# Optimization experiments

Measured on AMD Instinct MI355X. Metric: run time of the kernel, lower is better.

Reference implementation:

```python
import jax, jax.numpy as jnp
import numpy as np

B, C, H, W = 4, 512, 96, 96
NH = 8
HD = C // NH
NC = 128
D = 768
L = H * W
EPS = 1e-5  # torch LayerNorm default


def _l2n(x, axis):
    # F.normalize: x / max(||x||, 1e-12)
    return x / jnp.maximum(jnp.linalg.norm(x, axis=axis, keepdims=True), 1e-12)


def _ln2d(x, g, b):
    # LayerNorm2d: normalize over channel dim of (B,C,H,W)
    mu = x.mean(1, keepdims=True)
    var = ((x - mu) ** 2).mean(1, keepdims=True)
    return (x - mu) / jnp.sqrt(var + EPS) * g[None, :, None, None] + b[None, :, None, None]


def _conv1x1(x, w):
    return jnp.einsum('oc,bchw->bohw', w, x)


def setup_inputs() -> dict:
    key = jax.random.key(0)
    ks = jax.random.split(key, 9)
    s = 0.02
    return {
        'img_feats': jax.random.normal(ks[0], (B, C, H, W), jnp.float32),
        'cls_embs': jax.random.normal(ks[1], (NC, D), jnp.float32),
        'cls_logits': jax.random.normal(ks[2], (B, NC), jnp.float32),
        'seg_logits': jax.random.normal(ks[3], (B, 1, H, W), jnp.float32),
        'gamma_g': jnp.ones((D,), jnp.float32), 'beta_g': jnp.zeros((D,), jnp.float32),
        'gamma_f': jnp.ones((C,), jnp.float32), 'beta_f': jnp.zeros((C,), jnp.float32),
        'attn_scale': jnp.ones((NH, 1, 1), jnp.float32),
        'Wg': jax.random.normal(ks[4], (C, D), jnp.float32) * s,
        'Wqkv': jax.random.normal(ks[5], (3 * C, C), jnp.float32) * s,
        'Wo': jax.random.normal(ks[6], (C, C), jnp.float32) * s,
        'bo': jnp.zeros((C,), jnp.float32),
        'gamma_n': jnp.ones((C,), jnp.float32), 'beta_n': jnp.zeros((C,), jnp.float32),
        'W1': jax.random.normal(ks[7], (C, C), jnp.float32) * s, 'b1': jnp.zeros((C,), jnp.float32),
        'W2': jax.random.normal(ks[8], (C, C), jnp.float32) * s, 'b2': jnp.zeros((C,), jnp.float32),
    }


def reference(img_feats, cls_embs, cls_logits, seg_logits, gamma_g, beta_g,
              gamma_f, beta_f, attn_scale, Wg, Wqkv, Wo, bo, gamma_n, beta_n,
              W1, b1, W2, b2):
    xn = _ln2d(img_feats, gamma_f, beta_f)
    # guide LayerNorm over embedding dim
    mu = cls_embs.mean(-1, keepdims=True)
    var = ((cls_embs - mu) ** 2).mean(-1, keepdims=True)
    cn = (cls_embs - mu) / jnp.sqrt(var + EPS) * gamma_g + beta_g
    g = (cn @ Wg.T).reshape(NC, NH, HD)  # nc nh hd

    qkv = _conv1x1(xn, Wqkv).reshape(B, 3, NH, HD, L)
    q, k, v = qkv[:, 0], qkv[:, 1], qkv[:, 2]  # each (B,NH,HD,L)

    # cosine guide map + min-max normalization + softmax-weighted aggregation over classes
    gm = jnp.einsum('nhd,bhdl->bhnl', _l2n(g, -1), _l2n(q, -2))
    gm = gm - gm.min(-1, keepdims=True)
    gm = gm / gm.max(-1, keepdims=True)
    gm = (jax.nn.softmax(gm, axis=2) * gm).sum(2, keepdims=True)  # (B,NH,1,L)

    # auxiliary guide map from cls logits + masked pooling of k
    cls_obj = jnp.einsum('nhd,bn->bhd', g, cls_logits)
    mask = jax.nn.sigmoid(seg_logits)  # (B,1,H,W)
    seg_obj = (mask * k.reshape(B, C, H, W)).sum((2, 3)) / mask.sum((2, 3))  # (B,C)
    obj = _l2n(cls_obj + seg_obj.reshape(B, NH, HD), -1)
    aux = jnp.einsum('bhd,bhdl->bhl', obj, _l2n(k, -2))[:, :, None, :]
    aux = aux - aux.min(-1, keepdims=True)
    aux = aux / aux.max(-1, keepdims=True)
    gm = gm * aux

    v = gm * v
    # channel (transposed) cosine attention: (B,NH,HD,HD)
    attn = jnp.einsum('bhdl,bhel->bhde', _l2n(q, -1), _l2n(k, -1)) * attn_scale
    out = jnp.einsum('bhde,bhel->bhdl', jax.nn.softmax(attn, -1), v).reshape(B, C, H, W)

    x = img_feats + _conv1x1(out, Wo) + bo[None, :, None, None]
    # ConvMlp with pre-norm: LayerNorm2d -> 1x1 conv -> GELU -> 1x1 conv
    fin = _ln2d(x, gamma_n, beta_n)
    h = jax.nn.gelu(_conv1x1(fin, W1) + b1[None, :, None, None], approximate=False)
    return x + _conv1x1(h, W2) + b2[None, :, None, None]
```

## Files before the change

### kernel.cpp

```cpp
#include <hip/hip_runtime.h>
#include <hip/hip_bf16.h>
#include <math.h>

#define BB 4
#define CC 512
#define NHEAD 8
#define HDIM 64
#define NCLS 128
#define DD 768
#define LL 9216
#define BLPIX 36864
#define EPSV 1e-5f
#define GMBLK 144
#define AUXBLK 144
#define LSPLIT 8
#define NLT 72

typedef __hip_bfloat16 bf16;
typedef __attribute__((ext_vector_type(8))) short short8v;
typedef __attribute__((ext_vector_type(4))) short short4v;
typedef __attribute__((ext_vector_type(4))) float f32x4;

__device__ __forceinline__ float bf2f(bf16 v){ return __bfloat162float(v); }
__device__ __forceinline__ bf16 f2bf(float v){ return __float2bfloat16(v); }
__device__ __forceinline__ short bfbits(float v){ bf16 b = __float2bfloat16(v); return *reinterpret_cast<short*>(&b); }
__device__ __forceinline__ float s2f(short s){ bf16 b = *reinterpret_cast<bf16*>(&s); return __bfloat162float(b); }

__global__ __launch_bounds__(256) void wclsg_k(
    const float* __restrict__ wqkv, const float* __restrict__ wo,
    const float* __restrict__ w1, const float* __restrict__ w2,
    bf16* __restrict__ oq, bf16* __restrict__ oo,
    bf16* __restrict__ o1, bf16* __restrict__ o2,
    const float* __restrict__ cls_embs, const float* __restrict__ gamma_g,
    const float* __restrict__ beta_g, const float* __restrict__ Wg,
    float* __restrict__ g, bf16* __restrict__ gnb)
{
  __shared__ __align__(16) float cn[DD];
  __shared__ float red[256];
  __shared__ float gsh[CC];
  __shared__ float nrm[NHEAD];
  int bid = blockIdx.x;
  int tid = threadIdx.x;
  if (bid < 1536){
    int i = bid * 256 + tid;
    int e = i * 4;
    const float* src; bf16* dst; int off;
    if (e < 786432){ src = wqkv; dst = oq; off = e; }
    else if (e < 1048576){ src = wo; dst = oo; off = e - 786432; }
    else if (e < 1310720){ src = w1; dst = o1; off = e - 1048576; }
    else { src = w2; dst = o2; off = e - 1310720; }
    float4 v = *reinterpret_cast<const float4*>(src + off);
    short4v pk;
    pk[0] = bfbits(v.x); pk[1] = bfbits(v.y); pk[2] = bfbits(v.z); pk[3] = bfbits(v.w);
    *(short4v*)&dst[off] = pk;
    return;
  }
  {
    int n = bid - 1536;
    const float* e = cls_embs + (size_t)n * DD;
    float s = 0.f, ss = 0.f;
    for (int i = tid; i < DD; i += 256){ float v = e[i]; s += v; ss += v * v; }
    red[tid] = s; __syncthreads();
    for (int st = 128; st > 0; st >>= 1){ if (tid < st) red[tid] += red[tid + st]; __syncthreads(); }
    float mean = red[0] / DD; __syncthreads();
    red[tid] = ss; __syncthreads();
    for (int st = 128; st > 0; st >>= 1){ if (tid < st) red[tid] += red[tid + st]; __syncthreads(); }
    float var = red[0] / DD - mean * mean;
    float rstd = rsqrtf(var + EPSV);
    __syncthreads();
    for (int i = tid; i < DD; i += 256) cn[i] = (e[i] - mean) * rstd * gamma_g[i] + beta_g[i];
    __syncthreads();
    for (int c = tid; c < CC; c += 256){
      const float* w = Wg + (size_t)c * DD;
      float a = 0.f;
      #pragma unroll 8
      for (int d = 0; d < DD; d++) a += cn[d] * w[d];
      gsh[c] = a;
    }
    __syncthreads();
    if (tid < NHEAD){
      float a = 0.f;
      for (int d = 0; d < HDIM; d++){ float v = gsh[tid * HDIM + d]; a += v * v; }
      nrm[tid] = fmaxf(sqrtf(a), 1e-12f);
    }
    __syncthreads();
    for (int c = tid; c < CC; c += 256){
      g[(size_t)n * CC + c] = gsh[c];
      gnb[(size_t)n * CC + c] = f2bf(gsh[c] / nrm[c >> 6]);
    }
  }
}

__global__ __launch_bounds__(256) void fuse_ln_k(const float* __restrict__ X,
    const float* __restrict__ lng, const float* __restrict__ lnb,
    bf16* __restrict__ xnT){
  __shared__ float sred[2][4][64];
  __shared__ float muS[64], rsS[64];
  __shared__ float t[64][65];
  int p0 = blockIdx.x * 64;
  int b = p0 / LL, l0 = p0 - b * LL;
  int tid = threadIdx.x;
  int cg = tid >> 6, l = tid & 63;
  const float* base = X + (size_t)b * CC * LL + l0 + l;
  float s = 0.f, ss = 0.f;
  for (int c = cg * 128; c < cg * 128 + 128; c++){
    float v = base[(size_t)c * LL];
    s += v; ss += v * v;
  }
  sred[0][cg][l] = s; sred[1][cg][l] = ss;
  __syncthreads();
  if (tid < 64){
    float st = sred[0][0][tid] + sred[0][1][tid] + sred[0][2][tid] + sred[0][3][tid];
    float sst = sred[1][0][tid] + sred[1][1][tid] + sred[1][2][tid] + sred[1][3][tid];
    float m = st * (1.0f / CC);
    float var = sst * (1.0f / CC) - m * m;
    muS[tid] = m; rsS[tid] = rsqrtf(var + EPSV);
  }
  __syncthreads();
  int pr = tid >> 4;
  int cc = (tid & 15) * 4;
  for (int cb = 0; cb < 8; cb++){
    int c0 = cb * 64;
    #pragma unroll
    for (int i = 0; i < 16; i++){
      int idx = i * 256 + tid;
      int cl = idx >> 6, ll2 = idx & 63;
      t[cl][ll2] = X[(size_t)b * CC * LL + (size_t)(c0 + cl) * LL + l0 + ll2];
    }
    __syncthreads();
    #pragma unroll
    for (int i = 0; i < 4; i++){
      int pl = pr + i * 16;
      int p = p0 + pl;
      float m = muS[pl], r = rsS[pl];
      short4v pk;
      #pragma unroll
      for (int e = 0; e < 4; e++){
        int c = c0 + cc + e;
        pk[e] = bfbits((t[cc + e][pl] - m) * r * lng[c] + lnb[c]);
      }
      *(short4v*)&xnT[(size_t)p * CC + c0 + cc] = pk;
    }
    __syncthreads();
  }
}

__global__ __launch_bounds__(256) void qT_k(const bf16* __restrict__ q,
    bf16* __restrict__ qT, float* __restrict__ rq){
  __shared__ bf16 qs[64 * 68];
  __shared__ float sspart[4][64];
  int bh = blockIdx.x, lt = blockIdx.y;
  int l0 = lt * 64;
  int t = threadIdx.x;
  int b = bh >> 3, h = bh & 7;
  const bf16* qp = q + (size_t)b * CC * LL + (size_t)h * HDIM * LL + l0;
  #pragma unroll
  for (int i2 = 0; i2 < 4; i2++){
    int idx = t + i2 * 256;
    int d = idx >> 4, lch = (idx & 15) * 4;
    *(short4v*)&qs[d * 68 + lch] = *reinterpret_cast<const short4v*>(qp + (size_t)d * LL + lch);
  }
  __syncthreads();
  {
    int l = t & 63, dg = t >> 6;
    float ss = 0.f;
    #pragma unroll
    for (int dd = 0; dd < 16; dd++){ float v = bf2f(qs[(dg * 16 + dd) * 68 + l]); ss += v * v; }
    sspart[dg][l] = ss;
  }
  __syncthreads();
  if (t < 64){
    float ss = sspart[0][t] + sspart[1][t] + sspart[2][t] + sspart[3][t];
    rq[(size_t)bh * LL + l0 + t] = 1.0f / fmaxf(sqrtf(ss), 1e-12f);
  }
  int px = t >> 2, d0 = (t & 3) * 16;
  short8v o0, o1;
  #pragma unroll
  for (int jj = 0; jj < 8; jj++){
    o0[jj] = *reinterpret_cast<short*>(&qs[(d0 + jj) * 68 + px]);
    o1[jj] = *reinterpret_cast<short*>(&qs[(d0 + 8 + jj) * 68 + px]);
  }
  bf16* dst = qT + ((size_t)(b * LL + l0 + px)) * CC + h * 64 + d0;
  *(short8v*)dst = o0;
  *(short8v*)(dst + 8) = o1;
}

__global__ void statsred_k(const float2* __restrict__ statp, float* __restrict__ mu, float* __restrict__ rs){
  int p = blockIdx.x * 256 + threadIdx.x;
  if (p >= BLPIX) return;
  float s = 0.f, ss = 0.f;
  #pragma unroll
  for (int part = 0; part < 4; part++){
    float2 v = statp[part * BLPIX + p];
    s += v.x; ss += v.y;
  }
  float m = s * (1.0f / CC);
  float var = ss * (1.0f / CC) - m * m;
  mu[p] = m; rs[p] = rsqrtf(var + EPSV);
}

template<int MODE>
__global__ __launch_bounds__(256, 2) void mgemm_k(
    const bf16* __restrict__ A,
    const bf16* __restrict__ B,
    const float* __restrict__ residf,
    const bf16* __restrict__ residb,
    const float* __restrict__ bias,
    const float* __restrict__ mu, const float* __restrict__ rs,
    const float* __restrict__ lng, const float* __restrict__ lnb,
    float2* __restrict__ statp,
    float* __restrict__ qssp, float* __restrict__ kssp,
    bf16* __restrict__ qo, bf16* __restrict__ ko, bf16* __restrict__ vo,
    bf16* __restrict__ xT_out,
    float* __restrict__ xo,
    bf16* __restrict__ ho,
    const float* __restrict__ gA, const float* __restrict__ clsl, float* __restrict__ clsovO)
{
  __shared__ short Asm[128 * 64];
  __shared__ short Bsm[128 * 64];
  __shared__ float sredf[512];
  int tid = threadIdx.x;
  if (MODE == 0 && blockIdx.x >= 3456){
    int idx = (blockIdx.x - 3456) * 256 + tid;
    int b = idx >> 9, c = idx & 511;
    float a = 0.f;
    for (int n = 0; n < NCLS; n++) a += gA[(size_t)n * CC + c] * clsl[b * NCLS + n];
    clsovO[idx] = a;
    return;
  }
  int lane = tid & 63, wv = tid >> 6;
  int wr = wv >> 1, wc = wv & 1;
  int r15 = lane & 15, g = lane >> 4, h7 = lane & 7;
  int flat, gx, cpx;
  if (MODE == 0){ flat = blockIdx.x; gx = 12; cpx = 432; }
  else { gx = gridDim.x; flat = blockIdx.y * gx + blockIdx.x; cpx = (gx * gridDim.y) >> 3; }
  int swz = (flat & 7) * cpx + (flat >> 3);
  int m0 = (swz % gx) * 128, n0 = (swz / gx) * 128;
  int srow = tid >> 3, skkg = tid & 7;
  int sslot = ((skkg ^ (srow & 7))) * 8;

  f32x4 acc[4][4];
  #pragma unroll
  for (int i = 0; i < 4; i++)
    #pragma unroll
    for (int j = 0; j < 4; j++) acc[i][j] = (f32x4){0.f, 0.f, 0.f, 0.f};

  short8v pa[4], pb[4];
  auto loadAB = [&](int it){
    int k0 = it * 64;
    if (MODE == 2){
      int c0 = k0 + skkg * 8;
      float ga[8], be[8];
      *(float4*)&ga[0] = *(const float4*)&lng[c0];
      *(float4*)&ga[4] = *(const float4*)&lng[c0 + 4];
      *(float4*)&be[0] = *(const float4*)&lnb[c0];
      *(float4*)&be[4] = *(const float4*)&lnb[c0 + 4];
      #pragma unroll
      for (int r = 0; r < 4; r++){
        pa[r] = *reinterpret_cast<const short8v*>(A + (size_t)(m0 + r * 32 + srow) * 512 + c0);
        int rp = n0 + r * 32 + srow;
        float mm = mu[rp], rr = rs[rp];
        short8v rawv = *reinterpret_cast<const short8v*>(B + (size_t)rp * 512 + c0);
        short8v ov;
        #pragma unroll
        for (int e = 0; e < 8; e++){
          float v = (s2f(rawv[e]) - mm) * rr * ga[e] + be[e];
          ov[e] = bfbits(v);
        }
        pb[r] = ov;
      }
    } else {
      #pragma unroll
      for (int r = 0; r < 4; r++){
        pa[r] = *reinterpret_cast<const short8v*>(A + (size_t)(m0 + r * 32 + srow) * 512 + k0 + skkg * 8);
        pb[r] = *reinterpret_cast<const short8v*>(B + (size_t)(n0 + r * 32 + srow) * 512 + k0 + skkg * 8);
      }
    }
  };

  loadAB(0);
  for (int it = 0; it < 8; ++it){
    __syncthreads();
    #pragma unroll
    for (int r = 0; r < 4; r++){
      int row = r * 32 + srow;
      *(short8v*)&Asm[row * 64 + sslot] = pa[r];
      *(short8v*)&Bsm[row * 64 + sslot] = pb[r];
    }
    __syncthreads();
    if (it < 7) loadAB(it + 1);
    #pragma unroll
    for (int s = 0; s < 2; s++){
      int slot = ((s * 4 + g) ^ h7) * 8;
      short8v af[4], bf_[4];
      #pragma unroll
      for (int i = 0; i < 4; i++){
        af[i]  = *(const short8v*)&Asm[(wr * 64 + i * 16 + r15) * 64 + slot];
        bf_[i] = *(const short8v*)&Bsm[(wc * 64 + i * 16 + r15) * 64 + slot];
      }
      #pragma unroll
      for (int i = 0; i < 4; i++)
        #pragma unroll
        for (int j = 0; j < 4; j++){
          if (MODE == 2)
            acc[i][j] = __builtin_amdgcn_mfma_f32_16x16x32_bf16(bf_[i], af[j], acc[i][j], 0, 0, 0);
          else
            acc[i][j] = __builtin_amdgcn_mfma_f32_16x16x32_bf16(af[i], bf_[j], acc[i][j], 0, 0, 0);
        }
    }
  }

  int bIdx = n0 / LL;
  int lbase = n0 - bIdx * LL;
  if (MODE == 0){
    int part = m0 >> 9;
    if (part < 2){
      bf16* dst = (part == 0) ? qo : ko;
      int chb = (m0 & 511) + wr * 64;
      #pragma unroll
      for (int i = 0; i < 4; i++)
        #pragma unroll
        for (int j = 0; j < 4; j++){
          int l = lbase + wc * 64 + j * 16 + r15;
          #pragma unroll
          for (int e = 0; e < 4; e++){
            int ch = chb + i * 16 + g * 4 + e;
            dst[(size_t)bIdx * CC * LL + (size_t)ch * LL + l] = f2bf(acc[i][j][e]);
          }
        }
      #pragma unroll
      for (int i = 0; i < 4; i++)
        #pragma unroll
        for (int e = 0; e < 4; e++){
          float ssv = acc[i][0][e]*acc[i][0][e] + acc[i][1][e]*acc[i][1][e]
                    + acc[i][2][e]*acc[i][2][e] + acc[i][3][e]*acc[i][3][e];
          #pragma unroll
          for (int msk = 1; msk < 16; msk <<= 1) ssv += __shfl_xor(ssv, msk);
          if (r15 == 0) sredf[wv * 64 + i * 16 + g * 4 + e] = ssv;
        }
      __syncthreads();
      if (tid < 128){
        int wrr = tid >> 6, chL = tid & 63;
        float tot = sredf[(wrr * 2) * 64 + chL] + sredf[(wrr * 2 + 1) * 64 + chL];
        int c = (m0 & 511) + wrr * 64 + chL;
        int row = bIdx * 512 + c;
        int ltile = lbase >> 7;
        float* dd = (part == 0) ? qssp : kssp;
        dd[(size_t)row * NLT + ltile] = tot;
      }
    } else {
      int chb = (m0 & 511) + wr * 64;
      #pragma unroll
      for (int i = 0; i < 4; i++)
        #pragma unroll
        for (int j = 0; j < 4; j++){
          int l = lbase + wc * 64 + j * 16 + r15;
          int ch = chb + i * 16 + g * 4;
          short4v pk;
          #pragma unroll
          for (int e = 0; e < 4; e++) pk[e] = bfbits(acc[i][j][e]);
          *(short4v*)&vo[((size_t)bIdx * LL + l) * CC + ch] = pk;
        }
    }
  } else if (MODE == 1){
    float sj[4] = {0.f,0.f,0.f,0.f}, ssj[4] = {0.f,0.f,0.f,0.f};
    #pragma unroll
    for (int i = 0; i < 4; i++)
      #pragma unroll
      for (int j = 0; j < 4; j++){
        int l = lbase + wc * 64 + j * 16 + r15;
        int chm = m0 + wr * 64 + i * 16 + g * 4;
        short4v pk;
        #pragma unroll
        for (int e = 0; e < 4; e++){
          int m = chm + e;
          size_t o = (size_t)bIdx * CC * LL + (size_t)m * LL + l;
          float xv = residf[o] + acc[i][j][e] + bias[m];
          pk[e] = bfbits(xv);
          sj[j] += xv; ssj[j] += xv * xv;
        }
        *(short4v*)&xT_out[((size_t)bIdx * LL + l) * CC + chm] = pk;
      }
    #pragma unroll
    for (int j = 0; j < 4; j++){
      sj[j] += __shfl_xor(sj[j], 16); sj[j] += __shfl_xor(sj[j], 32);
      ssj[j] += __shfl_xor(ssj[j], 16); ssj[j] += __shfl_xor(ssj[j], 32);
    }
    if (g == 0){
      #pragma unroll
      for (int j = 0; j < 4; j++){
        sredf[wv * 128 + j * 32 + r15 * 2 + 0] = sj[j];
        sredf[wv * 128 + j * 32 + r15 * 2 + 1] = ssj[j];
      }
    }
    __syncthreads();
    if (tid < 128){
      int wv2 = tid >> 6, lane2 = tid & 63, j2 = lane2 >> 4, r2 = lane2 & 15;
      float s   = sredf[wv2 * 128 + j2 * 32 + r2 * 2 + 0] + sredf[(wv2 + 2) * 128 + j2 * 32 + r2 * 2 + 0];
      float ss2 = sredf[wv2 * 128 + j2 * 32 + r2 * 2 + 1] + sredf[(wv2 + 2) * 128 + j2 * 32 + r2 * 2 + 1];
      int p = n0 + wv2 * 64 + j2 * 16 + r2;
      statp[(m0 >> 7) * BLPIX + p] = make_float2(s, ss2);
    }
  } else if (MODE == 3){
    #pragma unroll
    for (int i = 0; i < 4; i++)
      #pragma unroll
      for (int j = 0; j < 4; j++){
        int l = lbase + wc * 64 + j * 16 + r15;
        int chm = m0 + wr * 64 + i * 16 + g * 4;
        short4v rv = *(const short4v*)&residb[((size_t)bIdx * LL + l) * CC + chm];
        #pragma unroll
        for (int e = 0; e < 4; e++){
          int m = chm + e;
          size_t o = (size_t)bIdx * CC * LL + (size_t)m * LL + l;
          xo[o] = s2f(rv[e]) + acc[i][j][e] + bias[m];
        }
      }
  } else {
    #pragma unroll
    for (int i = 0; i < 4; i++)
      #pragma unroll
      for (int j = 0; j < 4; j++){
        int mm = m0 + wr * 64 + j * 16 + r15;
        float bv = bias[mm];
        #pragma unroll
        for (int e = 0; e < 4; e++){
          int n = n0 + wc * 64 + i * 16 + g * 4 + e;
          float t = acc[i][j][e] + bv;
          float gv = 0.5f * t * (1.0f + erff(t * 0.70710678118654752f));
          ho[(size_t)n * CC + mm] = f2bf(gv);
        }
      }
  }
}

__global__ __launch_bounds__(256) void mega1_k(
    const bf16* __restrict__ q, const bf16* __restrict__ k, const bf16* __restrict__ gnb,
    const bf16* __restrict__ qT, const float* __restrict__ rq,
    float* __restrict__ pmin, float* __restrict__ pmax,
    float* __restrict__ part,
    const float* __restrict__ seg, float* __restrict__ seg_num, float* __restrict__ den,
    const float* __restrict__ qssp, const float* __restrict__ kssp,
    float* __restrict__ qn, float* __restrict__ kn)
{
  __shared__ __align__(16) float red[256];
  int bid = blockIdx.x;
  int t = threadIdx.x;
  if (bid < 4608){
    int bh = bid & 31, lt = bid >> 5;
    int l0 = lt * 64;
    int b = bh >> 3, h = bh & 7;
    int w = t >> 6, lane = t & 63, r15 = lane & 15, g = lane >> 4;
    short8v ag[2][2];
    #pragma unroll
    for (int i = 0; i < 2; i++)
      #pragma unroll
      for (int kt = 0; kt < 2; kt++)
        ag[i][kt] = *reinterpret_cast<const short8v*>(gnb + (size_t)(w * 32 + i * 16 + r15) * CC + h * 64 + kt * 32 + g * 8);
    const bf16* qTp = qT + ((size_t)(b * LL + l0)) * CC + h * 64;
    short8v bq[4][2];
    float rqv[4];
    #pragma unroll
    for (int j = 0; j < 4; j++){
      #pragma unroll
      for (int kt = 0; kt < 2; kt++)
        bq[j][kt] = *reinterpret_cast<const short8v*>(qTp + (size_t)(j * 16 + r15) * CC + kt * 32 + g * 8);
      rqv[j] = rq[(size_t)bh * LL + l0 + j * 16 + r15];
    }
    f32x4 acc[2][4];
    #pragma unroll
    for (int i = 0; i < 2; i++)
      #pragma unroll
      for (int j = 0; j < 4; j++) acc[i][j] = (f32x4){0.f,0.f,0.f,0.f};
    #pragma unroll
    for (int kt = 0; kt < 2; kt++)
      #pragma unroll
      for (int i = 0; i < 2; i++)
        #pragma unroll
        for (int j = 0; j < 4; j++)
          acc[i][j] = __builtin_amdgcn_mfma_f32_16x16x32_bf16(ag[i][kt], bq[j][kt], acc[i][j], 0, 0, 0);
    #pragma unroll
    for (int i = 0; i < 2; i++)
      #pragma unroll
      for (int e = 0; e < 4; e++){
        float mn = 1e30f, mx = -1e30f;
        #pragma unroll
        for (int j = 0; j < 4; j++){
          float v = acc[i][j][e] * rqv[j];
          mn = fminf(mn, v); mx = fmaxf(mx, v);
        }
        #pragma unroll
        for (int msk = 1; msk < 16; msk <<= 1){
          mn = fminf(mn, __shfl_xor(mn, msk));
          mx = fmaxf(mx, __shfl_xor(mx, msk));
        }
        if (r15 == 0){
          int n = w * 32 + i * 16 + g * 4 + e;
          pmin[((size_t)bh * 128 + n) * GMBLK + lt] = mn;
          pmax[((size_t)bh * 128 + n) * GMBLK + lt] = mx;
        }
      }
    return;
  }
  if (bid < 4864){
    int bid2 = bid - 4608;
    int ls = bid2 & 7, bh = bid2 >> 3;
    int b = bh >> 3, h = bh & 7;
    int w = t >> 6, lane = t & 63, r15 = lane & 15, g = lane >> 4;
    const bf16* qp = q + (size_t)b * CC * LL + (size_t)h * HDIM * LL;
    const bf16* kp = k + (size_t)b * CC * LL + (size_t)h * HDIM * LL;
    int kbase = ls * 1152;
    f32x4 acc4[4];
    #pragma unroll
    for (int j = 0; j < 4; j++) acc4[j] = (f32x4){0.f,0.f,0.f,0.f};
    for (int ks = 0; ks < 36; ks++){
      int koff = kbase + ks * 32 + g * 8;
      short8v aq = *reinterpret_cast<const short8v*>(qp + (size_t)(w * 16 + r15) * LL + koff);
      short8v bk[4];
      #pragma unroll
      for (int j = 0; j < 4; j++) bk[j] = *reinterpret_cast<const short8v*>(kp + (size_t)(j * 16 + r15) * LL + koff);
      #pragma unroll
      for (int j = 0; j < 4; j++)
        acc4[j] = __builtin_amdgcn_mfma_f32_16x16x32_bf16(aq, bk[j], acc4[j], 0, 0, 0);
    }
    #pragma unroll
    for (int j = 0; j < 4; j++)
      #pragma unroll
      for (int e = 0; e < 4; e++){
        int d = w * 16 + g * 4 + e;
        int ee = j * 16 + r15;
        part[((size_t)(bh * LSPLIT + ls)) * 4096 + d * 64 + ee] = acc4[j][e];
      }
    return;
  }
  if (bid < 6912){
    int bc = bid - 4864;
    int b = bc >> 9;
    const bf16* p = k + (size_t)bc * LL;
    const float* sp = seg + (size_t)b * LL;
    float s = 0.f;
    for (int i = t; i < LL; i += 256){
      float m = 1.0f / (1.0f + expf(-sp[i]));
      s += m * bf2f(p[i]);
    }
    red[t] = s; __syncthreads();
    for (int st = 128; st > 0; st >>= 1){ if (t < st) red[t] += red[t + st]; __syncthreads(); }
    if (t == 0) seg_num[bc] = red[0];
    return;
  }
  if (bid < 6916){
    int b = bid - 6912;
    const float* sp = seg + (size_t)b * LL;
    float s = 0.f;
    for (int i = t; i < LL; i += 256) s += 1.0f / (1.0f + expf(-sp[i]));
    red[t] = s; __syncthreads();
    for (int st = 128; st > 0; st >>= 1){ if (t < st) red[t] += red[t + st]; __syncthreads(); }
    if (t == 0) den[b] = red[0];
    return;
  }
  {
    int r4 = (bid - 6916) * 4 + (t >> 6);
    int lane = t & 63;
    const float* src = (r4 < 2048) ? qssp : kssp;
    int r = r4 & 2047;
    float s = src[(size_t)r * NLT + lane] + ((lane < 8) ? src[(size_t)r * NLT + 64 + lane] : 0.f);
    #pragma unroll
    for (int m = 1; m < 64; m <<= 1) s += __shfl_xor(s, m);
    if (lane == 0){
      float nv = fmaxf(sqrtf(s), 1e-12f);
      if (r4 < 2048) qn[r] = nv; else kn[r] = nv;
    }
  }
}

__global__ __launch_bounds__(256) void aux_k(const bf16* __restrict__ k,
                      const float* __restrict__ clsov, const float* __restrict__ segn,
                      const float* __restrict__ segd,
                      float* __restrict__ aux,
                      float* __restrict__ pmin, float* __restrict__ pmax){
  __shared__ bf16 ks[64 * 68];
  __shared__ float os[64];
  __shared__ float sspart[4][64], dotpart[4][64];
  int bh = blockIdx.x, lt = blockIdx.y;
  int l0 = lt * 64;
  int t = threadIdx.x;
  int b = bh >> 3, h = bh & 7;
  const bf16* kp = k + (size_t)b * CC * LL + (size_t)h * HDIM * LL + l0;
  #pragma unroll
  for (int i2 = 0; i2 < 4; i2++){
    int idx = t + i2 * 256;
    int d = idx >> 4, lch = (idx & 15) * 4;
    *(short4v*)&ks[d * 68 + lch] = *reinterpret_cast<const short4v*>(kp + (size_t)d * LL + lch);
  }
  if (t < 64){
    float sv = clsov[bh * 64 + t] + segn[bh * 64 + t] / segd[b];
    float ss2 = sv * sv;
    #pragma unroll
    for (int m = 1; m < 64; m <<= 1) ss2 += __shfl_xor(ss2, m);
    os[t] = sv / fmaxf(sqrtf(ss2), 1e-12f);
  }
  __syncthreads();
  {
    int dg = t >> 6, l = t & 63;
    float ssk = 0.f, dk = 0.f;
    #pragma unroll
    for (int dd = 0; dd < 16; dd++){
      float v = bf2f(ks[(dg * 16 + dd) * 68 + l]);
      ssk += v * v; dk += os[dg * 16 + dd] * v;
    }
    sspart[dg][l] = ssk; dotpart[dg][l] = dk;
  }
  __syncthreads();
  if (t < 64){
    float ss = sspart[0][t] + sspart[1][t] + sspart[2][t] + sspart[3][t];
    float dot = dotpart[0][t] + dotpart[1][t] + dotpart[2][t] + dotpart[3][t];
    float av = dot / fmaxf(sqrtf(ss), 1e-12f);
    aux[(size_t)bh * LL + l0 + t] = av;
    float mn = av, mx = av;
    #pragma unroll
    for (int m = 1; m < 64; m <<= 1){
      mn = fminf(mn, __shfl_xor(mn, m));
      mx = fmaxf(mx, __shfl_xor(mx, m));
    }
    if (t == 0){ pmin[bh * AUXBLK + lt] = mn; pmax[bh * AUXBLK + lt] = mx; }
  }
}

__global__ __launch_bounds__(256) void megared_k(
    const float* __restrict__ gpmin, const float* __restrict__ gpmax,
    float* __restrict__ gmin, float* __restrict__ gms,
    const float* __restrict__ apmin, const float* __restrict__ apmax,
    float* __restrict__ amin, float* __restrict__ ams,
    const float* __restrict__ part, const float* __restrict__ qn,
    const float* __restrict__ kn, const float* __restrict__ scale,
    bf16* __restrict__ Pb)
{
  __shared__ float As[64 * 65];
  int bid = blockIdx.x;
  int tid = threadIdx.x;
  if (bid < 1024){
    int row = bid * 4 + (tid >> 6);
    int lane = tid & 63;
    float mn = gpmin[(size_t)row * GMBLK + lane];
    float mx = gpmax[(size_t)row * GMBLK + lane];
    mn = fminf(mn, gpmin[(size_t)row * GMBLK + 64 + lane]);
    mx = fmaxf(mx, gpmax[(size_t)row * GMBLK + 64 + lane]);
    if (lane < 16){
      mn = fminf(mn, gpmin[(size_t)row * GMBLK + 128 + lane]);
      mx = fmaxf(mx, gpmax[(size_t)row * GMBLK + 128 + lane]);
    }
    #pragma unroll
    for (int m = 1; m < 64; m <<= 1){
      mn = fminf(mn, __shfl_xor(mn, m));
      mx = fmaxf(mx, __shfl_xor(mx, m));
    }
    if (lane == 0){ gmin[row] = mn; gms[row] = mx - mn; }
    return;
  }
  if (bid < 1032){
    int bh = (bid - 1024) * 4 + (tid >> 6);
    int lane = tid & 63;
    float mn = apmin[bh * AUXBLK + lane];
    float mx = apmax[bh * AUXBLK + lane];
    mn = fminf(mn, apmin[bh * AUXBLK + 64 + lane]);
    mx = fmaxf(mx, apmax[bh * AUXBLK + 64 + lane]);
    if (lane < 16){
      mn = fminf(mn, apmin[bh * AUXBLK + 128 + lane]);
      mx = fmaxf(mx, apmax[bh * AUXBLK + 128 + lane]);
    }
    #pragma unroll
    for (int m = 1; m < 64; m <<= 1){
      mn = fminf(mn, __shfl_xor(mn, m));
      mx = fmaxf(mx, __shfl_xor(mx, m));
    }
    if (lane == 0){ amin[bh] = mn; ams[bh] = mx - mn; }
    return;
  }
  {
    int bh = bid - 1032;
    int h = bh & 7;
    #pragma unroll
    for (int i = 0; i < 16; i++){
      int cell = tid + i * 256;
      int d = cell >> 6, e = cell & 63;
      float s = 0.f;
      #pragma unroll
      for (int ls = 0; ls < LSPLIT; ls++) s += part[((size_t)(bh * LSPLIT + ls)) * 4096 + cell];
      As[d * 65 + e] = s * scale[h] / (qn[bh * 64 + d] * kn[bh * 64 + e]);
    }
    __syncthreads();
    if (tid < 64){
      int d = tid;
      float mx = -1e30f;
      for (int e = 0; e < 64; e++) mx = fmaxf(mx, As[d * 65 + e]);
      float sum = 0.f;
      for (int e = 0; e < 64; e++){ float ev = expf(As[d * 65 + e] - mx); As[d * 65 + e] = ev; sum += ev; }
      float inv = 1.0f / sum;
      for (int e = 0; e < 64; e++) Pb[(size_t)bh * 4096 + d * 64 + e] = f2bf(As[d * 65 + e] * inv);
    }
  }
}

__global__ __launch_bounds__(256) void pv_k(const bf16* __restrict__ qT, const float* __restrict__ rq,
      const bf16* __restrict__ gnb,
      const float* __restrict__ aux,
      const float* __restrict__ gmin, const float* __restrict__ gms,
      const float* __restrict__ amin, const float* __restrict__ ams,
      const bf16* __restrict__ Pb, const bf16* __restrict__ vT, bf16* __restrict__ outT){
  __shared__ float gminS[128], rgmsS[128];
  __shared__ float separt[4][64], setpart[4][64];
  __shared__ float wl[64];
  int bh = blockIdx.x, lt = blockIdx.y;
  int l0 = lt * 64;
  int t = threadIdx.x;
  int b = bh >> 3, h = bh & 7;
  int w = t >> 6, lane = t & 63, r15 = lane & 15, g = lane >> 4;
  if (t < 128){ gminS[t] = gmin[bh * 128 + t]; rgmsS[t] = 1.0f / gms[bh * 128 + t]; }
  short8v ag[2][2];
  #pragma unroll
  for (int i = 0; i < 2; i++)
    #pragma unroll
    for (int kt = 0; kt < 2; kt++)
      ag[i][kt] = *reinterpret_cast<const short8v*>(gnb + (size_t)(w * 32 + i * 16 + r15) * CC + h * 64 + kt * 32 + g * 8);
  const bf16* qTp = qT + ((size_t)(b * LL + l0)) * CC + h * 64;
  short8v bq[4][2];
  float rqv[4];
  #pragma unroll
  for (int j = 0; j < 4; j++){
    #pragma unroll
    for (int kt = 0; kt < 2; kt++)
      bq[j][kt] = *reinterpret_cast<const short8v*>(qTp + (size_t)(j * 16 + r15) * CC + kt * 32 + g * 8);
    rqv[j] = rq[(size_t)bh * LL + l0 + j * 16 + r15];
  }
  f32x4 acc[2][4];
  #pragma unroll
  for (int i = 0; i < 2; i++)
    #pragma unroll
    for (int j = 0; j < 4; j++) acc[i][j] = (f32x4){0.f,0.f,0.f,0.f};
  #pragma unroll
  for (int kt = 0; kt < 2; kt++)
    #pragma unroll
    for (int i = 0; i < 2; i++)
      #pragma unroll
      for (int j = 0; j < 4; j++)
        acc[i][j] = __builtin_amdgcn_mfma_f32_16x16x32_bf16(ag[i][kt], bq[j][kt], acc[i][j], 0, 0, 0);
  __syncthreads();
  float seL[4] = {0.f,0.f,0.f,0.f}, setL[4] = {0.f,0.f,0.f,0.f};
  #pragma unroll
  for (int i = 0; i < 2; i++)
    #pragma unroll
    for (int j = 0; j < 4; j++)
      #pragma unroll
      for (int e = 0; e < 4; e++){
        int n = w * 32 + i * 16 + g * 4 + e;
        float tt = (acc[i][j][e] * rqv[j] - gminS[n]) * rgmsS[n];
        float ee = __expf(tt);
        seL[j] += ee; setL[j] += ee * tt;
      }
  #pragma unroll
  for (int j = 0; j < 4; j++){
    seL[j] += __shfl_xor(seL[j], 16); seL[j] += __shfl_xor(seL[j], 32);
    setL[j] += __shfl_xor(setL[j], 16); setL[j] += __shfl_xor(setL[j], 32);
  }
  if (g == 0){
    #pragma unroll
    for (int j = 0; j < 4; j++){ separt[w][j * 16 + r15] = seL[j]; setpart[w][j * 16 + r15] = setL[j]; }
  }
  __syncthreads();
  if (t < 64){
    float se = separt[0][t] + separt[1][t] + separt[2][t] + separt[3][t];
    float st = setpart[0][t] + setpart[1][t] + setpart[2][t] + setpart[3][t];
    float gmred = st / se;
    float auxn = (aux[(size_t)bh * LL + l0 + t] - amin[bh]) / ams[bh];
    wl[t] = gmred * auxn;
  }
  __syncthreads();
  short8v ap[4][2];
  #pragma unroll
  for (int i = 0; i < 4; i++)
    #pragma unroll
    for (int kt = 0; kt < 2; kt++)
      ap[i][kt] = *reinterpret_cast<const short8v*>(Pb + (size_t)bh * 4096 + (i * 16 + r15) * 64 + kt * 32 + g * 8);
  const bf16* vrow = vT + ((size_t)b * LL + l0 + w * 16 + r15) * CC + h * 64;
  short8v bv[2];
  #pragma unroll
  for (int kt = 0; kt < 2; kt++) bv[kt] = *reinterpret_cast<const short8v*>(vrow + kt * 32 + g * 8);
  f32x4 oacc[4];
  #pragma unroll
  for (int i = 0; i < 4; i++) oacc[i] = (f32x4){0.f,0.f,0.f,0.f};
  #pragma unroll
  for (int kt = 0; kt < 2; kt++)
    #pragma unroll
    for (int i = 0; i < 4; i++)
      oacc[i] = __builtin_amdgcn_mfma_f32_16x16x32_bf16(ap[i][kt], bv[kt], oacc[i], 0, 0, 0);
  float wlv = wl[w * 16 + r15];
  bf16* orow = outT + ((size_t)b * LL + l0 + w * 16 + r15) * CC + h * 64;
  #pragma unroll
  for (int i = 0; i < 4; i++){
    short4v pk;
    #pragma unroll
    for (int e = 0; e < 4; e++) pk[e] = bfbits(oacc[i][e] * wlv);
    *(short4v*)&orow[i * 16 + g * 4] = pk;
  }
}

extern "C" void kernel_launch(void* const* d_in, const int* in_sizes, int n_in,
                              void* d_out, int out_size, void* d_ws, size_t ws_size,
                              hipStream_t stream){
  const float* img        = (const float*)d_in[0];
  const float* cls_embs   = (const float*)d_in[1];
  const float* cls_logits = (const float*)d_in[2];
  const float* seg        = (const float*)d_in[3];
  const float* gamma_g    = (const float*)d_in[4];
  const float* beta_g     = (const float*)d_in[5];
  const float* gamma_f    = (const float*)d_in[6];
  const float* beta_f     = (const float*)d_in[7];
  const float* attn_scale = (const float*)d_in[8];
  const float* Wg         = (const float*)d_in[9];
  const float* Wqkv       = (const float*)d_in[10];
  const float* Wo         = (const float*)d_in[11];
  const float* bo         = (const float*)d_in[12];
  const float* gamma_n    = (const float*)d_in[13];
  const float* beta_n     = (const float*)d_in[14];
  const float* W1         = (const float*)d_in[15];
  const float* b1         = (const float*)d_in[16];
  const float* W2         = (const float*)d_in[17];
  const float* b2         = (const float*)d_in[18];
  float* outp = (float*)d_out;
  (void)in_sizes; (void)n_in; (void)out_size;

  char* wsb = (char*)d_ws;
  size_t off = 0;
  auto alloc = [&](size_t bytes)->char*{
    char* p = wsb + off;
    off += (bytes + 255) & ~(size_t)255;
    return p;
  };
  float* mu1   = (float*)alloc((size_t)BLPIX * 4);
  float* rs1   = (float*)alloc((size_t)BLPIX * 4);
  float2* statp= (float2*)alloc((size_t)4 * BLPIX * 8);
  float* qssp  = (float*)alloc((size_t)2048 * NLT * 4);
  float* kssp  = (float*)alloc((size_t)2048 * NLT * 4);
  float* qn    = (float*)alloc(2048 * 4);
  float* kn    = (float*)alloc(2048 * 4);
  float* rqb   = (float*)alloc((size_t)32 * LL * 4);
  float* gbuf  = (float*)alloc((size_t)NCLS * CC * 4);
  bf16*  gnbb  = (bf16*)alloc((size_t)NCLS * CC * 2);
  float* clsov = (float*)alloc(2048 * 4);
  float* segn  = (float*)alloc(2048 * 4);
  float* segd  = (float*)alloc(256);
  float* gminp = (float*)alloc((size_t)32 * 128 * GMBLK * 4);
  float* gmaxp = (float*)alloc((size_t)32 * 128 * GMBLK * 4);
  float* gminv = (float*)alloc(4096 * 4);
  float* gmsv  = (float*)alloc(4096 * 4);
  float* auxv  = (float*)alloc((size_t)32 * LL * 4);
  float* apmin = (float*)alloc(32 * AUXBLK * 4);
  float* apmax = (float*)alloc(32 * AUXBLK * 4);
  float* aminv = (float*)alloc(256);
  float* amsv  = (float*)alloc(256);
  bf16*  Pb    = (bf16*)alloc((size_t)32 * 4096 * 2);
  float* apart = (float*)alloc((size_t)32 * LSPLIT * 4096 * 4);
  bf16* qb    = (bf16*)alloc((size_t)BB * CC * LL * 2);
  bf16* kb    = (bf16*)alloc((size_t)BB * CC * LL * 2);
  bf16* wqkvb = (bf16*)alloc((size_t)1536 * 512 * 2);
  bf16* wob   = (bf16*)alloc((size_t)512 * 512 * 2);
  bf16* w1b   = (bf16*)alloc((size_t)512 * 512 * 2);
  bf16* w2b   = (bf16*)alloc((size_t)512 * 512 * 2);
  bf16* vT  = (bf16*)d_out;
  bf16* xnT = (bf16*)((char*)d_out + (size_t)BB * CC * LL * 2);
  bf16* qTb = xnT;
  bf16* outT = kb;
  bf16* xT   = qb;
  bf16* hbT  = kb;
  if (off > ws_size) return;

  wclsg_k<<<1664, 256, 0, stream>>>(Wqkv, Wo, W1, W2, wqkvb, wob, w1b, w2b,
      cls_embs, gamma_g, beta_g, Wg, gbuf, gnbb);
  fuse_ln_k<<<576, 256, 0, stream>>>(img, gamma_f, beta_f, xnT);
  mgemm_k<0><<<3464, 256, 0, stream>>>(wqkvb, xnT, nullptr, nullptr, nullptr,
      nullptr, nullptr, nullptr, nullptr, nullptr, qssp, kssp,
      qb, kb, vT, nullptr, nullptr, nullptr,
      gbuf, cls_logits, clsov);
  qT_k<<<dim3(32, 144), 256, 0, stream>>>(qb, qTb, rqb);
  mega1_k<<<7940, 256, 0, stream>>>(qb, kb, gnbb, qTb, rqb, gminp, gmaxp, apart,
      seg, segn, segd, qssp, kssp, qn, kn);
  aux_k<<<dim3(32, 144), 256, 0, stream>>>(kb, clsov, segn, segd, auxv, apmin, apmax);
  megared_k<<<1064, 256, 0, stream>>>(gminp, gmaxp, gminv, gmsv,
      apmin, apmax, aminv, amsv,
      apart, qn, kn, attn_scale, Pb);
  pv_k<<<dim3(32, GMBLK), 256, 0, stream>>>(qTb, rqb, gnbb, auxv, gminv, gmsv, aminv, amsv, Pb, vT, outT);
  mgemm_k<1><<<dim3(4, 288), 256, 0, stream>>>(wob, outT, img, nullptr, bo,
      nullptr, nullptr, nullptr, nullptr, statp, nullptr, nullptr,
      nullptr, nullptr, nullptr, xT, nullptr, nullptr,
      nullptr, nullptr, nullptr);
  statsred_k<<<144, 256, 0, stream>>>(statp, mu1, rs1);
  mgemm_k<2><<<dim3(4, 288), 256, 0, stream>>>(w1b, xT, nullptr, nullptr, b1,
      mu1, rs1, gamma_n, beta_n, nullptr, nullptr, nullptr,
      nullptr, nullptr, nullptr, nullptr, nullptr, hbT,
      nullptr, nullptr, nullptr);
  mgemm_k<3><<<dim3(4, 288), 256, 0, stream>>>(w2b, hbT, nullptr, xT, b2,
      nullptr, nullptr, nullptr, nullptr, nullptr, nullptr, nullptr,
      nullptr, nullptr, nullptr, nullptr, outp, nullptr,
      nullptr, nullptr, nullptr);
}
```

Before: 485.7 us.

## Fuse q transpose and row-norm into QKV GEMM epilogue, drop qT kernel

The QKV GEMM epilogue now writes q directly in pixel-major (transposed) layout and computes per-pixel inverse norms, so the separate transpose kernel and its extra read/write of q are removed. The q·k attention-gram blocks in mega1 now stage transposed q through shared memory instead of reading channel-major q. The guide-map blocks each process four L tiles to reuse the loaded guide fragments. The cost is more scattered stores in the GEMM epilogue and LDS transposes in the gram path.

```diff
diff --git a/kernel.cpp b/kernel.cpp
--- a/kernel.cpp
+++ b/kernel.cpp
@@ -145,46 +145,6 @@
   }
 }
 
-__global__ __launch_bounds__(256) void qT_k(const bf16* __restrict__ q,
-    bf16* __restrict__ qT, float* __restrict__ rq){
-  __shared__ bf16 qs[64 * 68];
-  __shared__ float sspart[4][64];
-  int bh = blockIdx.x, lt = blockIdx.y;
-  int l0 = lt * 64;
-  int t = threadIdx.x;
-  int b = bh >> 3, h = bh & 7;
-  const bf16* qp = q + (size_t)b * CC * LL + (size_t)h * HDIM * LL + l0;
-  #pragma unroll
-  for (int i2 = 0; i2 < 4; i2++){
-    int idx = t + i2 * 256;
-    int d = idx >> 4, lch = (idx & 15) * 4;
-    *(short4v*)&qs[d * 68 + lch] = *reinterpret_cast<const short4v*>(qp + (size_t)d * LL + lch);
-  }
-  __syncthreads();
-  {
-    int l = t & 63, dg = t >> 6;
-    float ss = 0.f;
-    #pragma unroll
-    for (int dd = 0; dd < 16; dd++){ float v = bf2f(qs[(dg * 16 + dd) * 68 + l]); ss += v * v; }
-    sspart[dg][l] = ss;
-  }
-  __syncthreads();
-  if (t < 64){
-    float ss = sspart[0][t] + sspart[1][t] + sspart[2][t] + sspart[3][t];
-    rq[(size_t)bh * LL + l0 + t] = 1.0f / fmaxf(sqrtf(ss), 1e-12f);
-  }
-  int px = t >> 2, d0 = (t & 3) * 16;
-  short8v o0, o1;
-  #pragma unroll
-  for (int jj = 0; jj < 8; jj++){
-    o0[jj] = *reinterpret_cast<short*>(&qs[(d0 + jj) * 68 + px]);
-    o1[jj] = *reinterpret_cast<short*>(&qs[(d0 + 8 + jj) * 68 + px]);
-  }
-  bf16* dst = qT + ((size_t)(b * LL + l0 + px)) * CC + h * 64 + d0;
-  *(short8v*)dst = o0;
-  *(short8v*)(dst + 8) = o1;
-}
-
 __global__ void statsred_k(const float2* __restrict__ statp, float* __restrict__ mu, float* __restrict__ rs){
   int p = blockIdx.x * 256 + threadIdx.x;
   if (p >= BLPIX) return;
@@ -210,7 +170,8 @@
     const float* __restrict__ lng, const float* __restrict__ lnb,
     float2* __restrict__ statp,
     float* __restrict__ qssp, float* __restrict__ kssp,
-    bf16* __restrict__ qo, bf16* __restrict__ ko, bf16* __restrict__ vo,
+    bf16* __restrict__ qTo, float* __restrict__ rqo,
+    bf16* __restrict__ ko, bf16* __restrict__ vo,
     bf16* __restrict__ xT_out,
     float* __restrict__ xo,
     bf16* __restrict__ ho,
@@ -314,8 +275,54 @@
   int lbase = n0 - bIdx * LL;
   if (MODE == 0){
     int part = m0 >> 9;
-    if (part < 2){
-      bf16* dst = (part == 0) ? qo : ko;
+    if (part == 0){
+      int chb = m0 + wr * 64;
+      #pragma unroll
+      for (int i = 0; i < 4; i++)
+        #pragma unroll
+        for (int j = 0; j < 4; j++){
+          int l = lbase + wc * 64 + j * 16 + r15;
+          int ch = chb + i * 16 + g * 4;
+          short4v pk;
+          #pragma unroll
+          for (int e = 0; e < 4; e++) pk[e] = bfbits(acc[i][j][e]);
+          *(short4v*)&qTo[((size_t)bIdx * LL + l) * CC + ch] = pk;
+        }
+      int head = chb >> 6;
+      int bh = bIdx * 8 + head;
+      #pragma unroll
+      for (int j = 0; j < 4; j++){
+        float ssl = 0.f;
+        #pragma unroll
+        for (int i = 0; i < 4; i++)
+          #pragma unroll
+          for (int e = 0; e < 4; e++) ssl += acc[i][j][e] * acc[i][j][e];
+        ssl += __shfl_xor(ssl, 16); ssl += __shfl_xor(ssl, 32);
+        if (g == 0){
+          int l = lbase + wc * 64 + j * 16 + r15;
+          rqo[(size_t)bh * LL + l] = 1.0f / fmaxf(sqrtf(ssl), 1e-12f);
+        }
+      }
+      #pragma unroll
+      for (int i = 0; i < 4; i++)
+        #pragma unroll
+        for (int e = 0; e < 4; e++){
+          float ssv = acc[i][0][e]*acc[i][0][e] + acc[i][1][e]*acc[i][1][e]
+                    + acc[i][2][e]*acc[i][2][e] + acc[i][3][e]*acc[i][3][e];
+          #pragma unroll
+          for (int msk = 1; msk < 16; msk <<= 1) ssv += __shfl_xor(ssv, msk);
+          if (r15 == 0) sredf[wv * 64 + i * 16 + g * 4 + e] = ssv;
+        }
+      __syncthreads();
+      if (tid < 128){
+        int wrr = tid >> 6, chL = tid & 63;
+        float tot = sredf[(wrr * 2) * 64 + chL] + sredf[(wrr * 2 + 1) * 64 + chL];
+        int c = m0 + wrr * 64 + chL;
+        int row = bIdx * 512 + c;
+        int ltile = lbase >> 7;
+        qssp[(size_t)row * NLT + ltile] = tot;
+      }
+    } else if (part == 1){
       int chb = (m0 & 511) + wr * 64;
       #pragma unroll
       for (int i = 0; i < 4; i++)
@@ -325,7 +332,7 @@
           #pragma unroll
           for (int e = 0; e < 4; e++){
             int ch = chb + i * 16 + g * 4 + e;
-            dst[(size_t)bIdx * CC * LL + (size_t)ch * LL + l] = f2bf(acc[i][j][e]);
+            ko[(size_t)bIdx * CC * LL + (size_t)ch * LL + l] = f2bf(acc[i][j][e]);
           }
         }
       #pragma unroll
@@ -345,8 +352,7 @@
         int c = (m0 & 511) + wrr * 64 + chL;
         int row = bIdx * 512 + c;
         int ltile = lbase >> 7;
-        float* dd = (part == 0) ? qssp : kssp;
-        dd[(size_t)row * NLT + ltile] = tot;
+        kssp[(size_t)row * NLT + ltile] = tot;
       }
     } else {
       int chb = (m0 & 511) + wr * 64;
@@ -435,20 +441,19 @@
 }
 
 __global__ __launch_bounds__(256) void mega1_k(
-    const bf16* __restrict__ q, const bf16* __restrict__ k, const bf16* __restrict__ gnb,
     const bf16* __restrict__ qT, const float* __restrict__ rq,
+    const bf16* __restrict__ k, const bf16* __restrict__ gnb,
     float* __restrict__ pmin, float* __restrict__ pmax,
     float* __restrict__ part,
     const float* __restrict__ seg, float* __restrict__ seg_num, float* __restrict__ den,
     const float* __restrict__ qssp, const float* __restrict__ kssp,
     float* __restrict__ qn, float* __restrict__ kn)
 {
-  __shared__ __align__(16) float red[256];
+  __shared__ __align__(16) bf16 qs[128 * 68];
   int bid = blockIdx.x;
   int t = threadIdx.x;
-  if (bid < 4608){
-    int bh = bid & 31, lt = bid >> 5;
-    int l0 = lt * 64;
+  if (bid < 1152){
+    int bh = bid & 31, ltg = bid >> 5;
     int b = bh >> 3, h = bh & 7;
     int w = t >> 6, lane = t & 63, r15 = lane & 15, g = lane >> 4;
     short8v ag[2][2];
@@ -457,71 +462,89 @@
       #pragma unroll
       for (int kt = 0; kt < 2; kt++)
         ag[i][kt] = *reinterpret_cast<const short8v*>(gnb + (size_t)(w * 32 + i * 16 + r15) * CC + h * 64 + kt * 32 + g * 8);
-    const bf16* qTp = qT + ((size_t)(b * LL + l0)) * CC + h * 64;
-    short8v bq[4][2];
-    float rqv[4];
-    #pragma unroll
-    for (int j = 0; j < 4; j++){
+    for (int sub = 0; sub < 4; sub++){
+      int lt = ltg * 4 + sub;
+      int l0 = lt * 64;
+      const bf16* qTp = qT + ((size_t)(b * LL + l0)) * CC + h * 64;
+      short8v bq[4][2];
+      float rqv[4];
+      #pragma unroll
+      for (int j = 0; j < 4; j++){
+        #pragma unroll
+        for (int kt = 0; kt < 2; kt++)
+          bq[j][kt] = *reinterpret_cast<const short8v*>(qTp + (size_t)(j * 16 + r15) * CC + kt * 32 + g * 8);
+        rqv[j] = rq[(size_t)bh * LL + l0 + j * 16 + r15];
+      }
+      f32x4 acc[2][4];
+      #pragma unroll
+      for (int i = 0; i < 2; i++)
+        #pragma unroll
+        for (int j = 0; j < 4; j++) acc[i][j] = (f32x4){0.f,0.f,0.f,0.f};
       #pragma unroll
       for (int kt = 0; kt < 2; kt++)
-        bq[j][kt] = *reinterpret_cast<const short8v*>(qTp + (size_t)(j * 16 + r15) * CC + kt * 32 + g * 8);
-      rqv[j] = rq[(size_t)bh * LL + l0 + j * 16 + r15];
-    }
-    f32x4 acc[2][4];
-    #pragma unroll
-    for (int i = 0; i < 2; i++)
-      #pragma unroll
-      for (int j = 0; j < 4; j++) acc[i][j] = (f32x4){0.f,0.f,0.f,0.f};
-    #pragma unroll
-    for (int kt = 0; kt < 2; kt++)
+        #pragma unroll
+        for (int i = 0; i < 2; i++)
+          #pragma unroll
+          for (int j = 0; j < 4; j++)
+            acc[i][j] = __builtin_amdgcn_mfma_f32_16x16x32_bf16(ag[i][kt], bq[j][kt], acc[i][j], 0, 0, 0);
       #pragma unroll
       for (int i = 0; i < 2; i++)
         #pragma unroll
-        for (int j = 0; j < 4; j++)
-          acc[i][j] = __builtin_amdgcn_mfma_f32_16x16x32_bf16(ag[i][kt], bq[j][kt], acc[i][j], 0, 0, 0);
-    #pragma unroll
-    for (int i = 0; i < 2; i++)
-      #pragma unroll
-      for (int e = 0; e < 4; e++){
-        float mn = 1e30f, mx = -1e30f;
-        #pragma unroll
-        for (int j = 0; j < 4; j++){
-          float v = acc[i][j][e] * rqv[j];
-          mn = fminf(mn, v); mx = fmaxf(mx, v);
-        }
-        #pragma unroll
-        for (int msk = 1; msk < 16; msk <<= 1){
-          mn = fminf(mn, __shfl_xor(mn, msk));
-          mx = fmaxf(mx, __shfl_xor(mx, msk));
-        }
-        if (r15 == 0){
-          int n = w * 32 + i * 16 + g * 4 + e;
-          pmin[((size_t)bh * 128 + n) * GMBLK + lt] = mn;
-          pmax[((size_t)bh * 128 + n) * GMBLK + lt] = mx;
-        }
-      }
+        for (int e = 0; e < 4; e++){
+          float mn = 1e30f, mx = -1e30f;
+          #pragma unroll
+          for (int j = 0; j < 4; j++){
+            float v = acc[i][j][e] * rqv[j];
+            mn = fminf(mn, v); mx = fmaxf(mx, v);
+          }
+          #pragma unroll
+          for (int msk = 1; msk < 16; msk <<= 1){
+            mn = fminf(mn, __shfl_xor(mn, msk));
+            mx = fmaxf(mx, __shfl_xor(mx, msk));
+          }
+          if (r15 == 0){
+            int n = w * 32 + i * 16 + g * 4 + e;
+            pmin[((size_t)bh * 128 + n) * GMBLK + lt] = mn;
+            pmax[((size_t)bh * 128 + n) * GMBLK + lt] = mx;
+          }
+        }
+    }
     return;
   }
-  if (bid < 4864){
-    int bid2 = bid - 4608;
+  if (bid < 1408){
+    int bid2 = bid - 1152;
     int ls = bid2 & 7, bh = bid2 >> 3;
     int b = bh >> 3, h = bh & 7;
     int w = t >> 6, lane = t & 63, r15 = lane & 15, g = lane >> 4;
-    const bf16* qp = q + (size_t)b * CC * LL + (size_t)h * HDIM * LL;
     const bf16* kp = k + (size_t)b * CC * LL + (size_t)h * HDIM * LL;
-    int kbase = ls * 1152;
     f32x4 acc4[4];
     #pragma unroll
     for (int j = 0; j < 4; j++) acc4[j] = (f32x4){0.f,0.f,0.f,0.f};
-    for (int ks = 0; ks < 36; ks++){
-      int koff = kbase + ks * 32 + g * 8;
-      short8v aq = *reinterpret_cast<const short8v*>(qp + (size_t)(w * 16 + r15) * LL + koff);
-      short8v bk[4];
-      #pragma unroll
-      for (int j = 0; j < 4; j++) bk[j] = *reinterpret_cast<const short8v*>(kp + (size_t)(j * 16 + r15) * LL + koff);
-      #pragma unroll
-      for (int j = 0; j < 4; j++)
-        acc4[j] = __builtin_amdgcn_mfma_f32_16x16x32_bf16(aq, bk[j], acc4[j], 0, 0, 0);
+    for (int stg = 0; stg < 9; stg++){
+      int lb = ls * 1152 + stg * 128;
+      #pragma unroll
+      for (int it = 0; it < 8; it++){
+        int idx = t + it * 256;
+        int row = idx >> 4, c4 = (idx & 15) * 4;
+        *(short4v*)&qs[row * 68 + c4] = *(const short4v*)&qT[((size_t)(b * LL + lb + row)) * CC + h * 64 + c4];
+      }
+      __syncthreads();
+      #pragma unroll
+      for (int kstep = 0; kstep < 4; kstep++){
+        int lloc = kstep * 32 + g * 8;
+        short8v aq;
+        #pragma unroll
+        for (int jj = 0; jj < 8; jj++)
+          aq[jj] = *reinterpret_cast<short*>(&qs[(lloc + jj) * 68 + w * 16 + r15]);
+        int koff = lb + kstep * 32 + g * 8;
+        short8v bk[4];
+        #pragma unroll
+        for (int j = 0; j < 4; j++) bk[j] = *reinterpret_cast<const short8v*>(kp + (size_t)(j * 16 + r15) * LL + koff);
+        #pragma unroll
+        for (int j = 0; j < 4; j++)
+          acc4[j] = __builtin_amdgcn_mfma_f32_16x16x32_bf16(aq, bk[j], acc4[j], 0, 0, 0);
+      }
+      __syncthreads();
     }
     #pragma unroll
     for (int j = 0; j < 4; j++)
@@ -533,8 +556,9 @@
       }
     return;
   }
-  if (bid < 6912){
-    int bc = bid - 4864;
+  if (bid < 3456){
+    float* red = (float*)qs;
+    int bc = bid - 1408;
     int b = bc >> 9;
     const bf16* p = k + (size_t)bc * LL;
     const float* sp = seg + (size_t)b * LL;
@@ -548,8 +572,9 @@
     if (t == 0) seg_num[bc] = red[0];
     return;
   }
-  if (bid < 6916){
-    int b = bid - 6912;
+  if (bid < 3460){
+    float* red = (float*)qs;
+    int b = bid - 3456;
     const float* sp = seg + (size_t)b * LL;
     float s = 0.f;
     for (int i = t; i < LL; i += 256) s += 1.0f / (1.0f + expf(-sp[i]));
@@ -559,7 +584,7 @@
     return;
   }
   {
-    int r4 = (bid - 6916) * 4 + (t >> 6);
+    int r4 = (bid - 3460) * 4 + (t >> 6);
     int lane = t & 63;
     const float* src = (r4 < 2048) ? qssp : kssp;
     int r = r4 & 2047;
@@ -868,7 +893,7 @@
   bf16* w2b   = (bf16*)alloc((size_t)512 * 512 * 2);
   bf16* vT  = (bf16*)d_out;
   bf16* xnT = (bf16*)((char*)d_out + (size_t)BB * CC * LL * 2);
-  bf16* qTb = xnT;
+  bf16* qTb = qb;
   bf16* outT = kb;
   bf16* xT   = qb;
   bf16* hbT  = kb;
@@ -879,10 +904,9 @@
   fuse_ln_k<<<576, 256, 0, stream>>>(img, gamma_f, beta_f, xnT);
   mgemm_k<0><<<3464, 256, 0, stream>>>(wqkvb, xnT, nullptr, nullptr, nullptr,
       nullptr, nullptr, nullptr, nullptr, nullptr, qssp, kssp,
-      qb, kb, vT, nullptr, nullptr, nullptr,
+      qTb, rqb, kb, vT, nullptr, nullptr, nullptr,
       gbuf, cls_logits, clsov);
-  qT_k<<<dim3(32, 144), 256, 0, stream>>>(qb, qTb, rqb);
-  mega1_k<<<7940, 256, 0, stream>>>(qb, kb, gnbb, qTb, rqb, gminp, gmaxp, apart,
+  mega1_k<<<4484, 256, 0, stream>>>(qTb, rqb, kb, gnbb, gminp, gmaxp, apart,
       seg, segn, segd, qssp, kssp, qn, kn);
   aux_k<<<dim3(32, 144), 256, 0, stream>>>(kb, clsov, segn, segd, auxv, apmin, apmax);
   megared_k<<<1064, 256, 0, stream>>>(gminp, gmaxp, gminv, gmsv,
@@ -891,15 +915,15 @@
   pv_k<<<dim3(32, GMBLK), 256, 0, stream>>>(qTb, rqb, gnbb, auxv, gminv, gmsv, aminv, amsv, Pb, vT, outT);
   mgemm_k<1><<<dim3(4, 288), 256, 0, stream>>>(wob, outT, img, nullptr, bo,
       nullptr, nullptr, nullptr, nullptr, statp, nullptr, nullptr,
-      nullptr, nullptr, nullptr, xT, nullptr, nullptr,
+      nullptr, nullptr, nullptr, nullptr, xT, nullptr, nullptr,
       nullptr, nullptr, nullptr);
   statsred_k<<<144, 256, 0, stream>>>(statp, mu1, rs1);
   mgemm_k<2><<<dim3(4, 288), 256, 0, stream>>>(w1b, xT, nullptr, nullptr, b1,
       mu1, rs1, gamma_n, beta_n, nullptr, nullptr, nullptr,
-      nullptr, nullptr, nullptr, nullptr, nullptr, hbT,
+      nullptr, nullptr, nullptr, nullptr, nullptr, nullptr, hbT,
       nullptr, nullptr, nullptr);
   mgemm_k<3><<<dim3(4, 288), 256, 0, stream>>>(w2b, hbT, nullptr, xT, b2,
       nullptr, nullptr, nullptr, nullptr, nullptr, nullptr, nullptr,
-      nullptr, nullptr, nullptr, nullptr, outp, nullptr,
+      nullptr, nullptr, nullptr, nullptr, nullptr, outp, nullptr,
       nullptr, nullptr, nullptr);
 }
```

Result: faster. 468.0 us (-3.6%).
